# Kernel tuning notes

Measured on AMD Instinct MI355X. Metric: run time of the kernel, lower is better.

Reference implementation:

```python
import jax, jax.numpy as jnp
import numpy as np

N_PIX = 32          # input image side
J = 2               # scattering scales
L = 8               # scattering angles
FEAT = 3 * 81 * 8 * 8   # 15552, flattened scattering features
RANK = 16
N_LAYERS = 2        # hidden LDR layers (plus one 'last' layer)
FFT_LEN = 32768     # >= 2*FEAT - 1, power of two
BN_EPS = 1e-5
NUM_CLASSES = 10


def _morlet_bank():
    """Morlet wavelet filter bank (Fourier domain) on the 32x32 periodic grid."""
    g = np.arange(N_PIX)
    g = np.where(g > N_PIX // 2, g - N_PIX, g).astype(np.float64)
    yy, xx = np.meshgrid(g, g, indexing='ij')
    r2 = xx ** 2 + yy ** 2
    psis = []
    for j in range(J):
        sigma = 0.8 * (2 ** j)
        xi = 3.0 * np.pi / 4.0 / (2 ** j)
        env = np.exp(-r2 / (2.0 * sigma ** 2))
        for l in range(L):
            theta = l * np.pi / L
            xr = xx * np.cos(theta) + yy * np.sin(theta)
            gab = env * np.exp(1j * xi * xr)
            K = gab.sum() / env.sum()   # make the wavelet zero-mean
            psis.append((gab - K * env) / (2.0 * np.pi * sigma ** 2))
    sig_phi = 0.8 * (2 ** J)
    phi = np.exp(-r2 / (2.0 * sig_phi ** 2)) / (2.0 * np.pi * sig_phi ** 2)
    psi_hat = np.fft.fft2(np.stack(psis))     # (2L, 32, 32) complex
    phi_hat = np.fft.fft2(phi)                # (32, 32) complex
    return (jnp.asarray(psi_hat, dtype=jnp.complex64),
            jnp.asarray(phi_hat, dtype=jnp.complex64))

PSI_HAT, PHI_HAT = _morlet_bank()


def _scattering(x):
    """Order-2 scattering transform: (B,3,32,32) -> (B,3,81,8,8)."""
    xh = jnp.fft.fft2(x.astype(jnp.complex64))                     # (B,3,32,32)
    # order 0: low-pass + subsample by 2^J = 4
    s0 = jnp.real(jnp.fft.ifft2(xh * PHI_HAT))[..., ::4, ::4][:, :, None]   # (B,3,1,8,8)
    # order 1: modulus of band-pass, then low-pass + subsample
    u1 = jnp.abs(jnp.fft.ifft2(xh[:, :, None] * PSI_HAT))          # (B,3,16,32,32)
    u1h = jnp.fft.fft2(u1.astype(jnp.complex64))
    s1 = jnp.real(jnp.fft.ifft2(u1h * PHI_HAT))[..., ::4, ::4]     # (B,3,16,8,8)
    # order 2: j1=0 paths (first L) through j2=1 wavelets (last L)
    u2 = jnp.abs(jnp.fft.ifft2(u1h[:, :, :L, None] * PSI_HAT[L:])) # (B,3,8,8,32,32)
    s2 = jnp.real(jnp.fft.ifft2(jnp.fft.fft2(u2.astype(jnp.complex64)) * PHI_HAT))[..., ::4, ::4]
    s2 = s2.reshape(s2.shape[0], s2.shape[1], L * L, 8, 8)         # (B,3,64,8,8)
    return jnp.concatenate([s0, s1, s2], axis=2)                   # (B,3,81,8,8)


def _ldr_subdiag(x, G, H, subd):
    """y = sum_i K(Z,g_i) K(Z,h_i)^T x, Z = subdiagonal shift (corner=False).
    K(Z,v)[m,j] = v[m-j] * P[m]/P[m-j] with P[k] = prod_{t<k} subd[t], so both
    Krylov products reduce to scaled causal (cross-)convolutions -> FFT.
    x: (B,n); G,H: (r,n); subd: (n-1,).
    """
    n = x.shape[-1]
    P = jnp.concatenate([jnp.ones((1,), x.dtype), jnp.cumprod(subd)])  # (n,)
    gh = G / P                       # (r,n) scaled generators
    hh = H / P
    a = x * P                        # (B,n)
    Af = jnp.fft.rfft(a, FFT_LEN)                                   # (B,F)
    Hf = jnp.fft.rfft(hh, FFT_LEN)                                  # (r,F)
    # c[b,i,j] = sum_k a[b,k] * hh[i,k-j]   (circular correlation, zero-padded)
    c = jnp.fft.irfft(Af[:, None] * jnp.conj(Hf), FFT_LEN)[..., :n] # (B,r,n)
    Gf = jnp.fft.rfft(gh, FFT_LEN)                                  # (r,F)
    Cf = jnp.fft.rfft(c, FFT_LEN)                                   # (B,r,F)
    y = jnp.fft.irfft(jnp.sum(Cf * Gf, axis=1), FFT_LEN)[..., :n]   # (B,n)
    return y * P


def setup_inputs() -> dict:
    key = jax.random.key(0)
    k0, k1, k2, k3 = jax.random.split(key, 4)
    B = 128
    x = jax.random.normal(k0, (B, 3, N_PIX, N_PIX), jnp.float32)
    # structured-nets init: G,H ~ N(0, 0.01^2); subdiag initialized at ones
    Gs = 0.01 * jax.random.normal(k1, (N_LAYERS + 1, RANK, FEAT), jnp.float32)
    Hs = 0.01 * jax.random.normal(k2, (N_LAYERS + 1, RANK, FEAT), jnp.float32)
    subds = 1.0 + 0.01 * jax.random.normal(k3, (N_LAYERS + 1, FEAT - 1), jnp.float32)
    return {
        'x': x,
        'bn_gamma': jnp.ones((FEAT,), jnp.float32),
        'bn_beta': jnp.zeros((FEAT,), jnp.float32),
        'Gs': Gs, 'Hs': Hs, 'subds': subds,
    }


def reference(x, bn_gamma, bn_beta, Gs, Hs, subds):
    f = _scattering(x).reshape(x.shape[0], -1)         # (B, 15552)
    mu = jnp.mean(f, axis=0)
    var = jnp.mean(jnp.square(f - mu), axis=0)         # biased var (train-mode BN)
    f = (f - mu) * jax.lax.rsqrt(var + BN_EPS) * bn_gamma + bn_beta
    f = jax.nn.relu(f)
    for l in range(N_LAYERS):
        f = jax.nn.relu(_ldr_subdiag(f, Gs[l], Hs[l], subds[l]))
    out = _ldr_subdiag(f, Gs[N_LAYERS], Hs[N_LAYERS], subds[N_LAYERS])
    return out[..., :NUM_CLASSES]
```

## Files before the change

kernel.cpp:

```cpp
#include <hip/hip_runtime.h>
#include <math.h>

#define NPIX 32
#define BATCH 128
#define NCH 3
#define NFEAT 15552
#define NHALF 7776
#define RANKR 16
#define MFFT 16384
#define MHALF 8192
#define NT 1024
#define PI_F 3.14159265358979323846f

__device__ __forceinline__ float2 cadd(float2 a, float2 b){ return make_float2(a.x+b.x, a.y+b.y); }
__device__ __forceinline__ float2 csub(float2 a, float2 b){ return make_float2(a.x-b.x, a.y-b.y); }
__device__ __forceinline__ float2 cmul(float2 a, float2 b){ return make_float2(a.x*b.x - a.y*b.y, a.x*b.y + a.y*b.x); }
__device__ __forceinline__ float2 cmulc(float2 a, float2 b){  return make_float2(a.x*b.x + a.y*b.y, a.y*b.x - a.x*b.y); }

__device__ __forceinline__ int swzi(int p){ return p ^ (((p>>4) ^ (p>>8)) & 15); }

__device__ __constant__ float TW32C[16] = {
  1.f, 0.98078528f, 0.92387953f, 0.83146961f,
  0.70710678f, 0.55557023f, 0.38268343f, 0.19509032f,
  0.f, -0.19509032f, -0.38268343f, -0.55557023f,
  -0.70710678f, -0.83146961f, -0.92387953f, -0.98078528f };
__device__ __constant__ float TW32S[16] = {
  0.f, -0.19509032f, -0.38268343f, -0.55557023f,
  -0.70710678f, -0.83146961f, -0.92387953f, -0.98078528f,
  -1.f, -0.98078528f, -0.92387953f, -0.83146961f,
  -0.70710678f, -0.55557023f, -0.38268343f, -0.19509032f };

__device__ __forceinline__ void fft32_fwd(float2* c){
  #pragma unroll
  for (int s = 4; s >= 0; --s){
    const int h = 1 << s;
    #pragma unroll
    for (int k = 0; k < 32; k += 2*h){
      #pragma unroll
      for (int j = 0; j < h; ++j){
        int i0 = k + j, i1 = i0 + h;
        float2 u = c[i0], v = c[i1];
        c[i0] = cadd(u, v);
        int e = j << (4 - s);
        float2 wt = make_float2(TW32C[e], TW32S[e]);
        c[i1] = cmul(csub(u, v), wt);
      }
    }
  }
}
__device__ __forceinline__ void fft32_inv(float2* c){
  #pragma unroll
  for (int s = 0; s <= 4; ++s){
    const int h = 1 << s;
    #pragma unroll
    for (int k = 0; k < 32; k += 2*h){
      #pragma unroll
      for (int j = 0; j < h; ++j){
        int i0 = k + j, i1 = i0 + h;
        int e = j << (4 - s);
        float2 wt = make_float2(TW32C[e], -TW32S[e]);
        float2 u = c[i0];
        float2 t = cmul(c[i1], wt);
        c[i0] = cadd(u, t);
        c[i1] = csub(u, t);
      }
    }
  }
}

template<bool INV>
__device__ __forceinline__ void fft2_lds(float2 (*A)[33], int tid, float scale){
  if (tid < 32){
    float2 c[32];
    #pragma unroll
    for (int e = 0; e < 32; ++e) c[e] = A[tid][e];
    if (INV) fft32_inv(c); else fft32_fwd(c);
    #pragma unroll
    for (int e = 0; e < 32; ++e) A[tid][e] = c[e];
  }
  __syncthreads();
  if (tid < 32){
    float2 c[32];
    #pragma unroll
    for (int e = 0; e < 32; ++e) c[e] = A[e][tid];
    if (INV) fft32_inv(c); else fft32_fwd(c);
    #pragma unroll
    for (int e = 0; e < 32; ++e) A[e][tid] = make_float2(c[e].x*scale, c[e].y*scale);
  }
  __syncthreads();
}

__global__ void k_twiddle(float2* __restrict__ tw, float2* __restrict__ tw2){
  int j = blockIdx.x*256 + threadIdx.x;
  if (j < MHALF){
    double a = -2.0 * 3.14159265358979323846 * (double)j / (double)MFFT;
    tw[j] = make_float2((float)cos(a), (float)sin(a));
  }
  if (j <= MHALF){
    double a = 3.14159265358979323846 * (double)j / (double)MFFT;
    tw2[j] = make_float2((float)cos(a), (float)sin(a));
  }
}

__device__ __forceinline__ int rev14(int f){ return (int)(__brev((unsigned)f) >> 18); }

__device__ __forceinline__ void fwd_quad(float2* z, const float2* __restrict__ tw, int s, int w){
  const int hq = 1 << (s-1);
  const int j = w & (hq - 1);
  const int i0 = ((w >> (s-1)) << (s+1)) + j;
  const int p0 = swzi(i0), p1 = swzi(i0+hq), p2 = swzi(i0+2*hq), p3 = swzi(i0+3*hq);
  float2 a0 = z[p0], a1 = z[p1], a2 = z[p2], a3 = z[p3];
  const int e1 = j << (13 - s);
  const float2 wA = tw[e1];
  const float2 wB = tw[e1 + 4096];
  const float2 wC = tw[j << (14 - s)];
  float2 t0 = cadd(a0, a2);
  float2 t2 = cmul(csub(a0, a2), wA);
  float2 t1 = cadd(a1, a3);
  float2 t3 = cmul(csub(a1, a3), wB);
  z[p0] = cadd(t0, t1);
  z[p1] = cmul(csub(t0, t1), wC);
  z[p2] = cadd(t2, t3);
  z[p3] = cmul(csub(t2, t3), wC);
}

__device__ __forceinline__ void inv_quad(float2* z, const float2* __restrict__ tw, int s, int w){
  const int h = 1 << s;
  const int j = w & (h - 1);
  const int i0 = ((w >> s) << (s + 2)) + j;
  const int p0 = swzi(i0), p1 = swzi(i0+h), p2 = swzi(i0+2*h), p3 = swzi(i0+3*h);
  float2 a0 = z[p0], a1 = z[p1], a2 = z[p2], a3 = z[p3];
  const int e1 = j << (13 - s);
  float2 wt = tw[e1]; wt.y = -wt.y;
  float2 m1 = cmul(a1, wt), m3 = cmul(a3, wt);
  float2 t0 = cadd(a0, m1), t1 = csub(a0, m1);
  float2 t2 = cadd(a2, m3), t3 = csub(a2, m3);
  const int e2 = j << (12 - s);
  float2 w0 = tw[e2]; w0.y = -w0.y;
  float2 w1 = tw[e2 + 4096]; w1.y = -w1.y;
  float2 u2 = cmul(t2, w0), u3 = cmul(t3, w1);
  z[p0] = cadd(t0, u2);
  z[p2] = csub(t0, u2);
  z[p1] = cadd(t1, u3);
  z[p3] = csub(t1, u3);
}

template<int SSTART, bool REGTAIL>
__device__ __forceinline__ void bigfft_fwd(float2* z, const float2* __restrict__ tw, int tid){
  #pragma unroll 1
  for (int s = SSTART; s >= (REGTAIL ? 5 : 3); s -= 2){
    #pragma unroll
    for (int wi = 0; wi < 4; ++wi) fwd_quad(z, tw, s, tid + wi*NT);
    __syncthreads();
  }
  if (REGTAIL){
    const int base = tid << 4;
    float2 c[16];
    #pragma unroll
    for (int r = 0; r < 16; ++r) c[r] = z[swzi(base + r)];
    #pragma unroll
    for (int s = 3; s >= 0; --s){
      const int h = 1 << s;
      #pragma unroll
      for (int k = 0; k < 16; k += 2*h){
        #pragma unroll
        for (int j = 0; j < h; ++j){
          const int i0 = k + j, i1 = i0 + h;
          float2 u = c[i0], v = c[i1];
          c[i0] = cadd(u, v);
          float2 wt = tw[j << (13 - s)];
          c[i1] = cmul(csub(u, v), wt);
        }
      }
    }
    #pragma unroll
    for (int r = 0; r < 16; ++r) z[swzi(base + r)] = c[r];
    __syncthreads();
  } else {
    #pragma unroll 2
    for (int wi = 0; wi < 4; ++wi){
      const int b4 = (tid + wi*NT) << 2;
      const int p0 = swzi(b4), p1 = swzi(b4+1), p2 = swzi(b4+2), p3 = swzi(b4+3);
      float2 e0 = z[p0], e1 = z[p1], e2 = z[p2], e3 = z[p3];
      float2 t0 = cadd(e0, e2), t2 = csub(e0, e2);
      float2 t1 = cadd(e1, e3);
      float2 d  = csub(e1, e3);
      float2 t3 = make_float2(d.y, -d.x);
      z[p0] = cadd(t0, t1);
      z[p1] = csub(t0, t1);
      z[p2] = cadd(t2, t3);
      z[p3] = csub(t2, t3);
    }
    __syncthreads();
  }
}

template<int SEND, bool REGTAIL>
__device__ __forceinline__ void bigfft_inv(float2* z, const float2* __restrict__ tw, int tid){
  if (REGTAIL){
    const int base = tid << 4;
    float2 c[16];
    #pragma unroll
    for (int r = 0; r < 16; ++r) c[r] = z[swzi(base + r)];
    #pragma unroll
    for (int s = 0; s <= 3; ++s){
      const int h = 1 << s;
      #pragma unroll
      for (int k = 0; k < 16; k += 2*h){
        #pragma unroll
        for (int j = 0; j < h; ++j){
          const int i0 = k + j, i1 = i0 + h;
          float2 wt = tw[j << (13 - s)]; wt.y = -wt.y;
          float2 u = c[i0];
          float2 t = cmul(c[i1], wt);
          c[i0] = cadd(u, t);
          c[i1] = csub(u, t);
        }
      }
    }
    #pragma unroll
    for (int r = 0; r < 16; ++r) z[swzi(base + r)] = c[r];
    __syncthreads();
  } else {
    #pragma unroll 2
    for (int wi = 0; wi < 4; ++wi){
      const int b4 = (tid + wi*NT) << 2;
      const int p0 = swzi(b4), p1 = swzi(b4+1), p2 = swzi(b4+2), p3 = swzi(b4+3);
      float2 c0 = z[p0], c1 = z[p1], c2 = z[p2], c3 = z[p3];
      float2 u0 = cadd(c0, c1), u1 = csub(c0, c1);
      float2 u2 = cadd(c2, c3), u3 = csub(c2, c3);
      float2 t  = make_float2(-u3.y, u3.x);
      z[p0] = cadd(u0, u2);
      z[p2] = csub(u0, u2);
      z[p1] = cadd(u1, t);
      z[p3] = csub(u1, t);
    }
    __syncthreads();
  }
  #pragma unroll 1
  for (int s = (REGTAIL ? 4 : 2); s <= SEND; s += 2){
    #pragma unroll
    for (int wi = 0; wi < 4; ++wi) inv_quad(z, tw, s, tid + wi*NT);
    __syncthreads();
  }
}

__device__ __forceinline__ void bigfft_mid_fused(float2* z, const float2* __restrict__ tw, int tid){
  #pragma unroll 2
  for (int wi = 0; wi < 4; ++wi){
    const int j = tid + wi*NT;
    const int p0 = swzi(j), p1 = swzi(j+4096), p2 = swzi(j+8192), p3 = swzi(j+12288);
    float2 a0 = z[p0], a1 = z[p1], a2 = z[p2], a3 = z[p3];
    float2 wt = tw[j<<1]; wt.y = -wt.y;
    float2 m1 = cmul(a1, wt), m3 = cmul(a3, wt);
    float2 t0 = cadd(a0, m1), t1 = csub(a0, m1);
    float2 t2 = cadd(a2, m3), t3 = csub(a2, m3);
    float2 w0 = tw[j]; w0.y = -w0.y;
    float2 w1 = tw[j+4096]; w1.y = -w1.y;
    float2 u2 = cmul(t2, w0), u3 = cmul(t3, w1);
    float2 c0 = cadd(t0, u2);
    float2 c1 = cadd(t1, u3);
    if (j + 4096 >= NHALF) c1 = make_float2(0.f, 0.f);
    const float2 wA = tw[j];
    const float2 wB = tw[j + 4096];
    const float2 wC = tw[j<<1];
    float2 t2f = cmul(c0, wA);
    float2 t3f = cmul(c1, wB);
    z[p0] = cadd(c0, c1);
    z[p1] = cmul(csub(c0, c1), wC);
    z[p2] = cadd(t2f, t3f);
    z[p3] = cmul(csub(t2f, t3f), wC);
  }
  __syncthreads();
}

template<typename F>
__device__ __forceinline__ void rfft_pack_f(float2* z, int tid, const float2* __restrict__ tw2, F Sget){
  #pragma unroll
  for (int k = 0; k < 8; ++k){
    int f = k*NT + tid;
    if (f == 0){
      float2 S0 = Sget(0), SM = Sget(MFFT);
      float2 E = make_float2(0.5f*(S0.x + SM.x), 0.5f*(S0.y - SM.y));
      float2 O = make_float2(0.5f*(S0.x - SM.x), 0.5f*(S0.y + SM.y));
      z[0] = make_float2(E.x - O.y, E.y + O.x);
    } else {
      float2 Sf = Sget(f), Sp = Sget(MFFT - f);
      float2 E = make_float2(0.5f*(Sf.x + Sp.x), 0.5f*(Sf.y - Sp.y));
      float2 D = make_float2(0.5f*(Sf.x - Sp.x), 0.5f*(Sf.y + Sp.y));
      float2 O = cmul(tw2[f], D);
      int pf = rev14(f), pp = rev14(MFFT - f);
      z[swzi(pf)] = make_float2(E.x - O.y,  E.y + O.x);
      z[swzi(pp)] = make_float2(E.x + O.y, -E.y + O.x);
    }
  }
  if (tid == 0){
    float2 S = Sget(MHALF);
    z[swzi(1)] = make_float2(S.x, -S.y);
  }
  __syncthreads();
}

__device__ __forceinline__ void rfft_unpack_store(const float2* z, int tid, const float2* __restrict__ tw2,
                                                  float2* __restrict__ out){
  #pragma unroll
  for (int k = 0; k < 8; ++k){
    int f = k*NT + tid;
    if (f == 0){
      float2 Z0 = z[0];
      out[0]    = make_float2(Z0.x + Z0.y, 0.f);
      out[MFFT] = make_float2(Z0.x - Z0.y, 0.f);
    } else {
      int pf = rev14(f), pp = rev14(MFFT - f);
      float2 Zf = z[swzi(pf)], Zp = z[swzi(pp)];
      float2 E = make_float2(0.5f*(Zf.x + Zp.x), 0.5f*(Zf.y - Zp.y));
      float2 Q = make_float2(0.5f*(Zf.x - Zp.x), 0.5f*(Zf.y + Zp.y));
      float2 O = make_float2(Q.y, -Q.x);
      float2 W = tw2[f];
      float2 T = cmul(make_float2(W.x, -W.y), O);
      out[f]        = make_float2(E.x + T.x, E.y + T.y);
      out[MFFT - f] = make_float2(E.x - T.x, T.y - E.y);
    }
  }
  if (tid == 0){
    float2 Zf = z[swzi(1)];
    out[MHALF] = make_float2(Zf.x, -Zf.y);
  }
}

__global__ void k_filters(float2* __restrict__ filt){
  int f = blockIdx.x;
  int tid = threadIdx.x;
  __shared__ float2 A[32][33];
  __shared__ float2 rg[64];
  __shared__ float  re_[64];
  bool isphi = (f == 16);
  float sigma, xi = 0.f, cth = 0.f, sth = 0.f;
  if (!isphi){
    int jj = f >> 3, l = f & 7;
    sigma = 0.8f * (float)(1 << jj);
    xi = 2.35619449019234f / (float)(1 << jj);
    float th = (float)l * 0.39269908169872414f;
    cth = cosf(th); sth = sinf(th);
  } else sigma = 3.2f;
  float inv2s2 = 1.f / (2.f * sigma * sigma);
  float norm = 1.f / (2.f * PI_F * sigma * sigma);
  float2 lg = make_float2(0.f, 0.f);
  float le = 0.f;
  for (int p = tid; p < 1024; p += 64){
    int iy = p >> 5, ix = p & 31;
    float gy = (iy > 16) ? (float)(iy - 32) : (float)iy;
    float gx = (ix > 16) ? (float)(ix - 32) : (float)ix;
    float r2 = gx*gx + gy*gy;
    float env = expf(-r2 * inv2s2);
    if (isphi){
      A[iy][ix] = make_float2(env * norm, 0.f);
    } else {
      float xr = gx*cth + gy*sth;
      float sn, cs; __sincosf(xi * xr, &sn, &cs);
      float2 gab = make_float2(env*cs, env*sn);
      A[iy][ix] = gab;
      lg = cadd(lg, gab);
      le += env;
    }
  }
  if (!isphi){
    rg[tid] = lg; re_[tid] = le;
    __syncthreads();
    for (int s = 32; s > 0; s >>= 1){
      if (tid < s){ rg[tid] = cadd(rg[tid], rg[tid+s]); re_[tid] += re_[tid+s]; }
      __syncthreads();
    }
    float2 K = make_float2(rg[0].x / re_[0], rg[0].y / re_[0]);
    for (int p = tid; p < 1024; p += 64){
      int iy = p >> 5, ix = p & 31;
      float gy = (iy > 16) ? (float)(iy - 32) : (float)iy;
      float gx = (ix > 16) ? (float)(ix - 32) : (float)ix;
      float r2 = gx*gx + gy*gy;
      float env = expf(-r2 * inv2s2);
      float2 v = A[iy][ix];
      A[iy][ix] = make_float2((v.x - K.x*env) * norm, (v.y - K.y*env) * norm);
    }
  }
  __syncthreads();
  fft2_lds<false>(A, tid, 1.f);
  for (int p = tid; p < 1024; p += 64)
    filt[(size_t)f*1024 + p] = A[p >> 5][p & 31];
}

__global__ void k_scat1(const float* __restrict__ x, const float2* __restrict__ filt,
                        float2* __restrict__ xh, float* __restrict__ feat){
  int bc = blockIdx.x, tid = threadIdx.x;
  int b = bc / 3, ch = bc % 3;
  __shared__ float2 A[32][33];
  for (int p = tid; p < 1024; p += 64)
    A[p>>5][p&31] = make_float2(x[(size_t)bc*1024 + p], 0.f);
  __syncthreads();
  fft2_lds<false>(A, tid, 1.f);
  const float2* phi = filt + 16*1024;
  for (int p = tid; p < 1024; p += 64){
    float2 v = A[p>>5][p&31];
    xh[(size_t)bc*1024 + p] = v;
    A[p>>5][p&31] = cmul(v, phi[p]);
  }
  __syncthreads();
  fft2_lds<true>(A, tid, 1.f/1024.f);
  int py = tid >> 3, px = tid & 7;
  feat[(size_t)b*NFEAT + ch*5184 + tid] = A[4*py][4*px].x;
}

__global__ void k_scat2(const float2* __restrict__ xh, const float2* __restrict__ filt,
                        float2* __restrict__ u1h, float* __restrict__ feat){
  int id = blockIdx.x, tid = threadIdx.x;
  int bc = id >> 4, l1 = id & 15;
  int b = bc / 3, ch = bc % 3;
  __shared__ float2 A[32][33];
  const float2* psi = filt + (size_t)l1*1024;
  for (int p = tid; p < 1024; p += 64)
    A[p>>5][p&31] = cmul(xh[(size_t)bc*1024 + p], psi[p]);
  __syncthreads();
  fft2_lds<true>(A, tid, 1.f/1024.f);
  for (int p = tid; p < 1024; p += 64){
    float2 v = A[p>>5][p&31];
    A[p>>5][p&31] = make_float2(sqrtf(v.x*v.x + v.y*v.y), 0.f);
  }
  __syncthreads();
  fft2_lds<false>(A, tid, 1.f);
  const float2* phi = filt + 16*1024;
  for (int p = tid; p < 1024; p += 64){
    float2 v = A[p>>5][p&31];
    if (l1 < 8) u1h[((size_t)bc*8 + l1)*1024 + p] = v;
    A[p>>5][p&31] = cmul(v, phi[p]);
  }
  __syncthreads();
  fft2_lds<true>(A, tid, 1.f/1024.f);
  int py = tid >> 3, px = tid & 7;
  feat[(size_t)b*NFEAT + ch*5184 + (1 + l1)*64 + tid] = A[4*py][4*px].x;
}

__global__ void k_scat3(const float2* __restrict__ u1h, const float2* __restrict__ filt,
                        float* __restrict__ feat){
  int id = blockIdx.x, tid = threadIdx.x;
  int l2 = id & 7; int rest = id >> 3;
  int l1 = rest & 7; int bc = rest >> 3;
  int b = bc / 3, ch = bc % 3;
  __shared__ float2 A[32][33];
  const float2* psi = filt + (size_t)(8 + l2)*1024;
  for (int p = tid; p < 1024; p += 64)
    A[p>>5][p&31] = cmul(u1h[(size_t)rest*1024 + p], psi[p]);
  __syncthreads();
  fft2_lds<true>(A, tid, 1.f/1024.f);
  for (int p = tid; p < 1024; p += 64){
    float2 v = A[p>>5][p&31];
    A[p>>5][p&31] = make_float2(sqrtf(v.x*v.x + v.y*v.y), 0.f);
  }
  __syncthreads();
  fft2_lds<false>(A, tid, 1.f);
  const float2* phi = filt + 16*1024;
  for (int p = tid; p < 1024; p += 64)
    A[p>>5][p&31] = cmul(A[p>>5][p&31], phi[p]);
  __syncthreads();
  fft2_lds<true>(A, tid, 1.f/1024.f);
  int py = tid >> 3, px = tid & 7;
  feat[(size_t)b*NFEAT + ch*5184 + (17 + l1*8 + l2)*64 + tid] = A[4*py][4*px].x;
}

__global__ void k_bn(float* __restrict__ feat, const float* __restrict__ gamma,
                     const float* __restrict__ beta){
  int k = blockIdx.x*256 + threadIdx.x;
  if (k >= NFEAT) return;
  float s = 0.f;
  for (int b = 0; b < BATCH; ++b) s += feat[(size_t)b*NFEAT + k];
  float mu = s * (1.f/BATCH);
  float v = 0.f;
  for (int b = 0; b < BATCH; ++b){ float d = feat[(size_t)b*NFEAT + k] - mu; v += d*d; }
  v *= (1.f/BATCH);
  float sc = rsqrtf(v + 1e-5f) * gamma[k];
  float bt = beta[k];
  for (int b = 0; b < BATCH; ++b){
    float val = (feat[(size_t)b*NFEAT + k] - mu) * sc + bt;
    feat[(size_t)b*NFEAT + k] = fmaxf(val, 0.f);
  }
}

__global__ __launch_bounds__(1024) void k_scan(const float* __restrict__ subd, float* __restrict__ P){
  __shared__ float ss[2][1024];
  int t = threadIdx.x;
  float loc[16];
  float prod = 1.f;
  #pragma unroll
  for (int r = 0; r < 16; ++r){
    int idx = t*16 + r;
    float v = (idx < NFEAT-1) ? subd[idx] : 1.f;
    prod *= v;
    loc[r] = prod;
  }
  int cur = 0;
  ss[0][t] = prod;
  __syncthreads();
  for (int offd = 1; offd < 1024; offd <<= 1){
    float v = ss[cur][t];
    if (t >= offd) v *= ss[cur][t - offd];
    ss[cur^1][t] = v;
    cur ^= 1;
    __syncthreads();
  }
  float excl = (t == 0) ? 1.f : ss[cur][t-1];
  #pragma unroll
  for (int r = 0; r < 16; ++r){
    int k = t*16 + r;
    if (k < NFEAT) P[k] = (r == 0) ? excl : excl * loc[r-1];
  }
}

__global__ __launch_bounds__(1024)
__attribute__((amdgpu_waves_per_eu(4, 4)))
void k_rfft_gh(const float* __restrict__ Gl, const float* __restrict__ Hl,
               const float* __restrict__ P, const float2* __restrict__ tw,
               const float2* __restrict__ tw2,
               float2* __restrict__ Gf, float2* __restrict__ Hf){
  int j = blockIdx.x, tid = threadIdx.x;
  const float* row = (j < 16) ? (Hl + (size_t)j*NFEAT) : (Gl + (size_t)(j-16)*NFEAT);
  float2* outp = (j < 16) ? (Hf + (size_t)j*(MFFT+1)) : (Gf + (size_t)(j-16)*(MFFT+1));
  __shared__ float2 z[MFFT + 16];
  for (int k = tid; k < MFFT; k += NT){
    float2 v = make_float2(0.f, 0.f);
    if (k < NHALF) v = make_float2(row[2*k]/P[2*k], row[2*k+1]/P[2*k+1]);
    z[swzi(k)] = v;
  }
  __syncthreads();
  bigfft_fwd<13, true>(z, tw, tid);
  rfft_unpack_store(z, tid, tw2, outp);
}

__global__ __launch_bounds__(1024)
__attribute__((amdgpu_waves_per_eu(4, 4)))
void k_rfft_a(const float* __restrict__ src, const float* __restrict__ P,
              const float2* __restrict__ tw, const float2* __restrict__ tw2,
              float2* __restrict__ Af){
  int b = blockIdx.x, tid = threadIdx.x;
  __shared__ float2 z[MFFT + 16];
  for (int k = tid; k < MFFT; k += NT){
    float2 v = make_float2(0.f, 0.f);
    if (k < NHALF){
      size_t i = (size_t)b*NFEAT + 2*k;
      v = make_float2(src[i]*P[2*k], src[i+1]*P[2*k+1]);
    }
    z[swzi(k)] = v;
  }
  __syncthreads();
  bigfft_fwd<13, true>(z, tw, tid);
  rfft_unpack_store(z, tid, tw2, Af + (size_t)b*(MFFT+1));
}

__global__ __launch_bounds__(1024)
__attribute__((amdgpu_waves_per_eu(4, 4)))
void k_main(const float2* __restrict__ Af, const float2* __restrict__ Hf,
            const float2* __restrict__ Gf, const float2* __restrict__ tw,
            const float2* __restrict__ tw2, float2* __restrict__ Yp){
  int x = blockIdx.x & 7, jj = blockIdx.x >> 3;
  int b = x*16 + (jj >> 1), half = jj & 1;
  int tid = threadIdx.x;
  __shared__ float2 z[MFFT + 16];
  float2 accA[8], accB[8];
  #pragma unroll
  for (int r = 0; r < 8; ++r){ accA[r] = make_float2(0.f,0.f); accB[r] = make_float2(0.f,0.f); }
  float2 accC = make_float2(0.f, 0.f);
  const float2* Ab = Af + (size_t)b*(MFFT+1);
  for (int ii = 0; ii < 8; ++ii){
    int i = half*8 + ii;
    const float2* Hi = Hf + (size_t)i*(MFFT+1);
    const float2* Gi = Gf + (size_t)i*(MFFT+1);
    rfft_pack_f(z, tid, tw2, [&](int f){ return cmulc(Ab[f], Hi[f]); });
    bigfft_inv<10, false>(z, tw, tid);
    bigfft_mid_fused(z, tw, tid);
    bigfft_fwd<11, false>(z, tw, tid);
    #pragma unroll
    for (int k = 0; k < 8; ++k){
      int f = k*NT + tid;
      if (f == 0){
        float2 Z0 = z[0];
        accA[0] = cadd(accA[0], cmul(make_float2(Z0.x + Z0.y, 0.f), Gi[0]));
        accB[0] = cadd(accB[0], cmul(make_float2(Z0.x - Z0.y, 0.f), Gi[MFFT]));
      } else {
        int pf = rev14(f), pp = rev14(MFFT - f);
        float2 Zf = z[swzi(pf)], Zp = z[swzi(pp)];
        float2 E = make_float2(0.5f*(Zf.x + Zp.x), 0.5f*(Zf.y - Zp.y));
        float2 Q = make_float2(0.5f*(Zf.x - Zp.x), 0.5f*(Zf.y + Zp.y));
        float2 O = make_float2(Q.y, -Q.x);
        float2 W = tw2[f];
        float2 T = cmul(make_float2(W.x, -W.y), O);
        float2 Sf = make_float2(E.x + T.x, E.y + T.y);
        float2 Sm = make_float2(E.x - T.x, T.y - E.y);
        accA[k] = cadd(accA[k], cmul(Sf, Gi[f]));
        accB[k] = cadd(accB[k], cmul(Sm, Gi[MFFT - f]));
      }
    }
    if (tid == 0){
      float2 Zf = z[swzi(1)];
      accC = cadd(accC, cmul(make_float2(Zf.x, -Zf.y), Gi[MHALF]));
    }
    __syncthreads();
  }
  float2* Yb = Yp + ((size_t)half*BATCH + b)*(MFFT+1);
  #pragma unroll
  for (int k = 0; k < 8; ++k){
    int f = k*NT + tid;
    if (f == 0){
      Yb[0]    = accA[0];
      Yb[MFFT] = accB[0];
    } else {
      Yb[f]        = accA[k];
      Yb[MFFT - f] = accB[k];
    }
  }
  if (tid == 0) Yb[MHALF] = accC;
}

__global__ __launch_bounds__(1024)
__attribute__((amdgpu_waves_per_eu(4, 4)))
void k_fin(const float2* __restrict__ Yp, const float* __restrict__ P,
           const float2* __restrict__ tw, const float2* __restrict__ tw2,
           float* __restrict__ dst, int relu){
  int b = blockIdx.x, tid = threadIdx.x;
  __shared__ float2 z[MFFT + 16];
  const float2* Y0 = Yp + (size_t)b*(MFFT+1);
  const float2* Y1 = Yp + ((size_t)BATCH + b)*(MFFT+1);
  rfft_pack_f(z, tid, tw2, [&](int f){ return cadd(Y0[f], Y1[f]); });
  bigfft_inv<12, true>(z, tw, tid);
  const float s = 1.f / ((float)MFFT * (float)MFFT);
  for (int k = tid; k < NHALF; k += NT){
    float2 v = z[swzi(k)];
    float y0 = v.x * s * P[2*k];
    float y1 = v.y * s * P[2*k+1];
    if (relu){ y0 = fmaxf(y0, 0.f); y1 = fmaxf(y1, 0.f); }
    dst[(size_t)b*NFEAT + 2*k]     = y0;
    dst[(size_t)b*NFEAT + 2*k + 1] = y1;
  }
}

__global__ void k_wlast(const float* __restrict__ G2, const float* __restrict__ H2,
                        const float* __restrict__ P, float* __restrict__ Wl){
  int k = blockIdx.x*256 + threadIdx.x;
  if (k >= NFEAT) return;
  float Pk = P[k];
  for (int t = 0; t < 10; ++t){
    float s = 0.f;
    int jmax = (t < k) ? t : k;
    for (int i = 0; i < RANKR; ++i){
      const float* g = G2 + (size_t)i*NFEAT;
      const float* h = H2 + (size_t)i*NFEAT;
      for (int j = 0; j <= jmax; ++j){
        s += (g[t-j] * h[k-j]) / (P[t-j] * P[k-j]);
      }
    }
    Wl[(size_t)t*NFEAT + k] = P[t] * Pk * s;
  }
}

__global__ void k_out(const float* __restrict__ f, const float* __restrict__ Wl,
                      float* __restrict__ out){
  int b = blockIdx.x, tid = threadIdx.x;
  float acc[10];
  #pragma unroll
  for (int t = 0; t < 10; ++t) acc[t] = 0.f;
  for (int k = tid; k < NFEAT; k += 256){
    float fv = f[(size_t)b*NFEAT + k];
    #pragma unroll
    for (int t = 0; t < 10; ++t) acc[t] += fv * Wl[(size_t)t*NFEAT + k];
  }
  __shared__ float red[10][256];
  #pragma unroll
  for (int t = 0; t < 10; ++t) red[t][tid] = acc[t];
  __syncthreads();
  for (int s = 128; s > 0; s >>= 1){
    if (tid < s){
      #pragma unroll
      for (int t = 0; t < 10; ++t) red[t][tid] += red[t][tid + s];
    }
    __syncthreads();
  }
  if (tid < 10) out[(size_t)b*10 + tid] = red[tid][0];
}

extern "C" void kernel_launch(void* const* d_in, const int* in_sizes, int n_in,
                              void* d_out, int out_size, void* d_ws, size_t ws_size,
                              hipStream_t stream){
  (void)in_sizes; (void)n_in; (void)out_size; (void)ws_size;
  const float* x     = (const float*)d_in[0];
  const float* gamma = (const float*)d_in[1];
  const float* beta  = (const float*)d_in[2];
  const float* Gs    = (const float*)d_in[3];
  const float* Hs    = (const float*)d_in[4];
  const float* subds = (const float*)d_in[5];
  float* out = (float*)d_out;

  char* base = (char*)d_ws;
  size_t off = 0;
  auto alloc = [&](size_t bytes) -> char* {
    char* p = base + off;
    off += (bytes + 255) & ~(size_t)255;
    return p;
  };
  float2* tw   = (float2*)alloc(MHALF * sizeof(float2));
  float2* tw2  = (float2*)alloc((MHALF + 1) * sizeof(float2));
  float2* filt = (float2*)alloc(17 * 1024 * sizeof(float2));
  float*  feat = (float*)alloc((size_t)BATCH * NFEAT * sizeof(float));
  float*  ybuf = (float*)alloc((size_t)BATCH * NFEAT * sizeof(float));
  float*  P    = (float*)alloc(NFEAT * sizeof(float));
  float*  Wl   = (float*)alloc(10 * NFEAT * sizeof(float));
  char* R = alloc(54529280);
  float2* xh  = (float2*)R;
  float2* u1h = (float2*)(R + 3145728);
  float2* Af  = (float2*)R;
  float2* Yp  = (float2*)(R + 16778240);
  float2* Gf  = (float2*)(R + 16778240 + 33556480);
  float2* Hf  = (float2*)(R + 16778240 + 33556480 + 2097280);

  k_twiddle<<<33, 256, 0, stream>>>(tw, tw2);
  k_filters<<<17, 64, 0, stream>>>(filt);
  k_scat1<<<BATCH*NCH, 64, 0, stream>>>(x, filt, xh, feat);
  k_scat2<<<BATCH*NCH*16, 64, 0, stream>>>(xh, filt, u1h, feat);
  k_scat3<<<BATCH*NCH*64, 64, 0, stream>>>(u1h, filt, feat);
  k_bn<<<(NFEAT+255)/256, 256, 0, stream>>>(feat, gamma, beta);

  for (int l = 0; l < 2; ++l){
    const float* src = (l == 0) ? feat : ybuf;
    float* dst = (l == 0) ? ybuf : feat;
    k_scan<<<1, 1024, 0, stream>>>(subds + (size_t)l*(NFEAT-1), P);
    k_rfft_gh<<<32, 1024, 0, stream>>>(Gs + (size_t)l*RANKR*NFEAT, Hs + (size_t)l*RANKR*NFEAT, P, tw, tw2, Gf, Hf);
    k_rfft_a<<<BATCH, 1024, 0, stream>>>(src, P, tw, tw2, Af);
    k_main<<<BATCH*2, 1024, 0, stream>>>(Af, Hf, Gf, tw, tw2, Yp);
    k_fin<<<BATCH, 1024, 0, stream>>>(Yp, P, tw, tw2, dst, 1);
  }

  k_scan<<<1, 1024, 0, stream>>>(subds + (size_t)2*(NFEAT-1), P);
  k_wlast<<<(NFEAT+255)/256, 256, 0, stream>>>(Gs + (size_t)2*RANKR*NFEAT, Hs + (size_t)2*RANKR*NFEAT, P, Wl);
  k_out<<<BATCH, 256, 0, stream>>>(feat, Wl, out);
}
```

Baseline: 1.968 ms.

## Park k_main accumulators in AGPRs and use register radix-16 FFT tails everywhere

Moves the 34 per-thread frequency accumulators in k_main into accumulation registers via inline v_accvgpr read/write, which frees VGPRs for the FFT stages. The small FFTs in k_main now use the 16-point in-register tail instead of the shared-memory radix-4 tail, removing one LDS pass and one barrier per FFT. The mid-stage loop is fully unrolled and the waves_per_eu(4,4) attributes are dropped. The risks are extra register pressure from the larger register tail and the cost of moving values in and out of AGPRs through inline asm.

Result: slower. 2.042 ms (+3.8%).

```diff
diff --git a/kernel.cpp b/kernel.cpp
--- a/kernel.cpp
+++ b/kernel.cpp
@@ -16,6 +16,15 @@
 __device__ __forceinline__ float2 csub(float2 a, float2 b){ return make_float2(a.x-b.x, a.y-b.y); }
 __device__ __forceinline__ float2 cmul(float2 a, float2 b){ return make_float2(a.x*b.x - a.y*b.y, a.x*b.y + a.y*b.x); }
 __device__ __forceinline__ float2 cmulc(float2 a, float2 b){  return make_float2(a.x*b.x + a.y*b.y, a.y*b.x - a.x*b.y); }
+
+__device__ __forceinline__ void agpr_w(float& slot, float v){
+  asm volatile("v_accvgpr_write_b32 %0, %1" : "=a"(slot) : "v"(v));
+}
+__device__ __forceinline__ float agpr_r(float& slot){
+  float v;
+  asm volatile("v_accvgpr_read_b32 %0, %1" : "=v"(v) : "a"(slot));
+  return v;
+}
 
 __device__ __forceinline__ int swzi(int p){ return p ^ (((p>>4) ^ (p>>8)) & 15); }
 
@@ -145,15 +154,15 @@
   z[p3] = csub(t1, u3);
 }
 
-template<int SSTART, bool REGTAIL>
+template<int SSTART>
 __device__ __forceinline__ void bigfft_fwd(float2* z, const float2* __restrict__ tw, int tid){
   #pragma unroll 1
-  for (int s = SSTART; s >= (REGTAIL ? 5 : 3); s -= 2){
+  for (int s = SSTART; s >= 5; s -= 2){
     #pragma unroll
     for (int wi = 0; wi < 4; ++wi) fwd_quad(z, tw, s, tid + wi*NT);
     __syncthreads();
   }
-  if (REGTAIL){
+  {
     const int base = tid << 4;
     float2 c[16];
     #pragma unroll
@@ -175,29 +184,13 @@
     }
     #pragma unroll
     for (int r = 0; r < 16; ++r) z[swzi(base + r)] = c[r];
-    __syncthreads();
-  } else {
-    #pragma unroll 2
-    for (int wi = 0; wi < 4; ++wi){
-      const int b4 = (tid + wi*NT) << 2;
-      const int p0 = swzi(b4), p1 = swzi(b4+1), p2 = swzi(b4+2), p3 = swzi(b4+3);
-      float2 e0 = z[p0], e1 = z[p1], e2 = z[p2], e3 = z[p3];
-      float2 t0 = cadd(e0, e2), t2 = csub(e0, e2);
-      float2 t1 = cadd(e1, e3);
-      float2 d  = csub(e1, e3);
-      float2 t3 = make_float2(d.y, -d.x);
-      z[p0] = cadd(t0, t1);
-      z[p1] = csub(t0, t1);
-      z[p2] = cadd(t2, t3);
-      z[p3] = csub(t2, t3);
-    }
-    __syncthreads();
-  }
-}
-
-template<int SEND, bool REGTAIL>
+  }
+  __syncthreads();
+}
+
+template<int SEND>
 __device__ __forceinline__ void bigfft_inv(float2* z, const float2* __restrict__ tw, int tid){
-  if (REGTAIL){
+  {
     const int base = tid << 4;
     float2 c[16];
     #pragma unroll
@@ -220,25 +213,10 @@
     }
     #pragma unroll
     for (int r = 0; r < 16; ++r) z[swzi(base + r)] = c[r];
-    __syncthreads();
-  } else {
-    #pragma unroll 2
-    for (int wi = 0; wi < 4; ++wi){
-      const int b4 = (tid + wi*NT) << 2;
-      const int p0 = swzi(b4), p1 = swzi(b4+1), p2 = swzi(b4+2), p3 = swzi(b4+3);
-      float2 c0 = z[p0], c1 = z[p1], c2 = z[p2], c3 = z[p3];
-      float2 u0 = cadd(c0, c1), u1 = csub(c0, c1);
-      float2 u2 = cadd(c2, c3), u3 = csub(c2, c3);
-      float2 t  = make_float2(-u3.y, u3.x);
-      z[p0] = cadd(u0, u2);
-      z[p2] = csub(u0, u2);
-      z[p1] = cadd(u1, t);
-      z[p3] = csub(u1, t);
-    }
-    __syncthreads();
-  }
+  }
+  __syncthreads();
   #pragma unroll 1
-  for (int s = (REGTAIL ? 4 : 2); s <= SEND; s += 2){
+  for (int s = 4; s <= SEND; s += 2){
     #pragma unroll
     for (int wi = 0; wi < 4; ++wi) inv_quad(z, tw, s, tid + wi*NT);
     __syncthreads();
@@ -246,7 +224,7 @@
 }
 
 __device__ __forceinline__ void bigfft_mid_fused(float2* z, const float2* __restrict__ tw, int tid){
-  #pragma unroll 2
+  #pragma unroll
   for (int wi = 0; wi < 4; ++wi){
     const int j = tid + wi*NT;
     const int p0 = swzi(j), p1 = swzi(j+4096), p2 = swzi(j+8192), p3 = swzi(j+12288);
@@ -514,7 +492,6 @@
 }
 
 __global__ __launch_bounds__(1024)
-__attribute__((amdgpu_waves_per_eu(4, 4)))
 void k_rfft_gh(const float* __restrict__ Gl, const float* __restrict__ Hl,
                const float* __restrict__ P, const float2* __restrict__ tw,
                const float2* __restrict__ tw2,
@@ -529,12 +506,11 @@
     z[swzi(k)] = v;
   }
   __syncthreads();
-  bigfft_fwd<13, true>(z, tw, tid);
+  bigfft_fwd<13>(z, tw, tid);
   rfft_unpack_store(z, tid, tw2, outp);
 }
 
 __global__ __launch_bounds__(1024)
-__attribute__((amdgpu_waves_per_eu(4, 4)))
 void k_rfft_a(const float* __restrict__ src, const float* __restrict__ P,
               const float2* __restrict__ tw, const float2* __restrict__ tw2,
               float2* __restrict__ Af){
@@ -549,12 +525,11 @@
     z[swzi(k)] = v;
   }
   __syncthreads();
-  bigfft_fwd<13, true>(z, tw, tid);
+  bigfft_fwd<13>(z, tw, tid);
   rfft_unpack_store(z, tid, tw2, Af + (size_t)b*(MFFT+1));
 }
 
 __global__ __launch_bounds__(1024)
-__attribute__((amdgpu_waves_per_eu(4, 4)))
 void k_main(const float2* __restrict__ Af, const float2* __restrict__ Hf,
             const float2* __restrict__ Gf, const float2* __restrict__ tw,
             const float2* __restrict__ tw2, float2* __restrict__ Yp){
@@ -562,26 +537,30 @@
   int b = x*16 + (jj >> 1), half = jj & 1;
   int tid = threadIdx.x;
   __shared__ float2 z[MFFT + 16];
-  float2 accA[8], accB[8];
-  #pragma unroll
-  for (int r = 0; r < 8; ++r){ accA[r] = make_float2(0.f,0.f); accB[r] = make_float2(0.f,0.f); }
-  float2 accC = make_float2(0.f, 0.f);
+  float aAx[8], aAy[8], aBx[8], aBy[8], aCx, aCy;
+  #pragma unroll
+  for (int r = 0; r < 8; ++r){
+    agpr_w(aAx[r], 0.f); agpr_w(aAy[r], 0.f);
+    agpr_w(aBx[r], 0.f); agpr_w(aBy[r], 0.f);
+  }
+  agpr_w(aCx, 0.f); agpr_w(aCy, 0.f);
   const float2* Ab = Af + (size_t)b*(MFFT+1);
   for (int ii = 0; ii < 8; ++ii){
     int i = half*8 + ii;
     const float2* Hi = Hf + (size_t)i*(MFFT+1);
     const float2* Gi = Gf + (size_t)i*(MFFT+1);
     rfft_pack_f(z, tid, tw2, [&](int f){ return cmulc(Ab[f], Hi[f]); });
-    bigfft_inv<10, false>(z, tw, tid);
+    bigfft_inv<10>(z, tw, tid);
     bigfft_mid_fused(z, tw, tid);
-    bigfft_fwd<11, false>(z, tw, tid);
+    bigfft_fwd<11>(z, tw, tid);
     #pragma unroll
     for (int k = 0; k < 8; ++k){
       int f = k*NT + tid;
+      float2 dA, dB;
       if (f == 0){
         float2 Z0 = z[0];
-        accA[0] = cadd(accA[0], cmul(make_float2(Z0.x + Z0.y, 0.f), Gi[0]));
-        accB[0] = cadd(accB[0], cmul(make_float2(Z0.x - Z0.y, 0.f), Gi[MFFT]));
+        dA = cmul(make_float2(Z0.x + Z0.y, 0.f), Gi[0]);
+        dB = cmul(make_float2(Z0.x - Z0.y, 0.f), Gi[MFFT]);
       } else {
         int pf = rev14(f), pp = rev14(MFFT - f);
         float2 Zf = z[swzi(pf)], Zp = z[swzi(pp)];
@@ -592,13 +571,19 @@
         float2 T = cmul(make_float2(W.x, -W.y), O);
         float2 Sf = make_float2(E.x + T.x, E.y + T.y);
         float2 Sm = make_float2(E.x - T.x, T.y - E.y);
-        accA[k] = cadd(accA[k], cmul(Sf, Gi[f]));
-        accB[k] = cadd(accB[k], cmul(Sm, Gi[MFFT - f]));
+        dA = cmul(Sf, Gi[f]);
+        dB = cmul(Sm, Gi[MFFT - f]);
       }
+      agpr_w(aAx[k], agpr_r(aAx[k]) + dA.x);
+      agpr_w(aAy[k], agpr_r(aAy[k]) + dA.y);
+      agpr_w(aBx[k], agpr_r(aBx[k]) + dB.x);
+      agpr_w(aBy[k], agpr_r(aBy[k]) + dB.y);
     }
     if (tid == 0){
       float2 Zf = z[swzi(1)];
-      accC = cadd(accC, cmul(make_float2(Zf.x, -Zf.y), Gi[MHALF]));
+      float2 dC = cmul(make_float2(Zf.x, -Zf.y), Gi[MHALF]);
+      agpr_w(aCx, agpr_r(aCx) + dC.x);
+      agpr_w(aCy, agpr_r(aCy) + dC.y);
     }
     __syncthreads();
   }
@@ -606,19 +591,20 @@
   #pragma unroll
   for (int k = 0; k < 8; ++k){
     int f = k*NT + tid;
+    float2 vA = make_float2(agpr_r(aAx[k]), agpr_r(aAy[k]));
+    float2 vB = make_float2(agpr_r(aBx[k]), agpr_r(aBy[k]));
     if (f == 0){
-      Yb[0]    = accA[0];
-      Yb[MFFT] = accB[0];
+      Yb[0]    = vA;
+      Yb[MFFT] = vB;
     } else {
-      Yb[f]        = accA[k];
-      Yb[MFFT - f] = accB[k];
-    }
-  }
-  if (tid == 0) Yb[MHALF] = accC;
+      Yb[f]        = vA;
+      Yb[MFFT - f] = vB;
+    }
+  }
+  if (tid == 0) Yb[MHALF] = make_float2(agpr_r(aCx), agpr_r(aCy));
 }
 
 __global__ __launch_bounds__(1024)
-__attribute__((amdgpu_waves_per_eu(4, 4)))
 void k_fin(const float2* __restrict__ Yp, const float* __restrict__ P,
            const float2* __restrict__ tw, const float2* __restrict__ tw2,
            float* __restrict__ dst, int relu){
@@ -627,7 +613,7 @@
   const float2* Y0 = Yp + (size_t)b*(MFFT+1);
   const float2* Y1 = Yp + ((size_t)BATCH + b)*(MFFT+1);
   rfft_pack_f(z, tid, tw2, [&](int f){ return cadd(Y0[f], Y1[f]); });
-  bigfft_inv<12, true>(z, tw, tid);
+  bigfft_inv<12>(z, tw, tid);
   const float s = 1.f / ((float)MFFT * (float)MFFT);
   for (int k = tid; k < NHALF; k += NT){
     float2 v = z[swzi(k)];
```
